# Kernel optimization log

Measured on AMD Instinct MI355X. Metric: run time of the kernel, lower is better.

Reference implementation:

```python
import jax, jax.numpy as jnp
import numpy as np

B, L, D, H = 2, 2048, 1024, 16
Dh = D // H


def setup_inputs() -> dict:
    key = jax.random.key(0)
    k = jax.random.split(key, 6)
    s = 1.0 / np.sqrt(D).astype(np.float32)
    return {
        "x": jax.random.normal(k[0], (B, L, D), jnp.float32),
        "mask": jnp.ones((B, L), jnp.int32),
        "user_emb": jax.random.normal(k[1], (B, D), jnp.float32),
        "W_q": jax.random.normal(k[2], (D, D), jnp.float32) * s,
        "W_k": jax.random.normal(k[3], (D, D), jnp.float32) * s,
        "W_v": jax.random.normal(k[4], (D, D), jnp.float32) * s,
        "W_o": jax.random.normal(k[5], (D, D), jnp.float32) * s,
    }


def reference(x, mask, user_emb, W_q, W_k, W_v, W_o):
    b, l, d = x.shape
    # torch nn.Linear(bias=False): y = x @ W.T
    Q = x @ W_q.T
    K = x @ W_k.T
    V = x @ W_v.T

    def split(t):  # [B,L,D] -> [B,H,L,Dh]
        return t.reshape(b, l, H, Dh).transpose(0, 2, 1, 3)

    Qh, Kh, Vh = split(Q), split(K), split(V)

    # additive_bias: rank-1 per-head user bias, [B,H,L,1]
    u = user_emb.reshape(b, H, Dh)
    bias = jnp.einsum('bhld,bhd->bhl', Qh, u)[..., None]

    scores = jnp.einsum('bhld,bhmd->bhlm', Qh, Kh) / np.float32(np.sqrt(Dh))
    scores = scores + bias
    # padding mask: 1 = valid, 0 = pad (broadcast over query dim)
    scores = jnp.where(mask[:, None, None, :] == 0, -jnp.inf, scores)
    # causal mask
    causal = jnp.triu(jnp.ones((l, l), jnp.bool_), k=1)
    scores = jnp.where(causal, -jnp.inf, scores)

    attn = jax.nn.softmax(scores, axis=-1)  # dropout p=0 -> identity
    ctx = jnp.einsum('bhlm,bhmd->bhld', attn, Vh)
    out = ctx.transpose(0, 2, 1, 3).reshape(b, l, d)
    return out @ W_o.T
```

## Files before the change

### kernel.cpp

```cpp
#include <hip/hip_runtime.h>
#include <hip/hip_bf16.h>
#include <stdint.h>

#define Bc 2
#define Lc 2048
#define Dc 1024
#define Hc 16
#define DHc 64

using f32x4  = __attribute__((ext_vector_type(4))) float;
using f32x16 = __attribute__((ext_vector_type(16))) float;
using bf16x8 = __attribute__((ext_vector_type(8))) short;
using bf16x4 = __attribute__((ext_vector_type(4))) short;

static __device__ __forceinline__ unsigned short f2bf(float f) {
  __hip_bfloat16 h = __float2bfloat16(f);
  return __builtin_bit_cast(unsigned short, h);
}
static __device__ __forceinline__ float bf2f(unsigned short u) {
  unsigned int x = ((unsigned int)u) << 16;
  return __builtin_bit_cast(float, x);
}
static __device__ __forceinline__ unsigned int cvtpk(float a, float b) {
  unsigned int r;
  asm("v_cvt_pk_bf16_f32 %0, %1, %2" : "=v"(r) : "v"(a), "v"(b));
  return r;
}

static __device__ __forceinline__ void gload16(const void* g, void* l) {
  __builtin_amdgcn_global_load_lds(
      (const __attribute__((address_space(1))) unsigned int*)g,
      (__attribute__((address_space(3))) unsigned int*)l, 16, 0, 0);
}

__global__ __launch_bounds__(256) void cvt_kernel(
    const float* __restrict__ x,  const float* __restrict__ wq,
    const float* __restrict__ wk, const float* __restrict__ wv,
    const float* __restrict__ wo,
    unsigned short* __restrict__ xb,  unsigned short* __restrict__ wqb,
    unsigned short* __restrict__ wkb, unsigned short* __restrict__ wvb,
    unsigned short* __restrict__ wob) {
  int i = (blockIdx.x * 256 + threadIdx.x) * 4;
  const float* src; unsigned short* dst; int off;
  if (i < 4194304) { src = x; dst = xb; off = i; }
  else {
    int j = i - 4194304; int w = j >> 20; off = j & 1048575;
    src = w == 0 ? wq : w == 1 ? wk : w == 2 ? wv : wo;
    dst = w == 0 ? wqb : w == 1 ? wkb : w == 2 ? wvb : wob;
  }
  float4 v = *(const float4*)(src + off);
  ushort4 u;
  u.x = f2bf(v.x); u.y = f2bf(v.y); u.z = f2bf(v.z); u.w = f2bf(v.w);
  *(ushort4*)(dst + off) = u;
}

__global__ __launch_bounds__(512) void gemm_qkv256(
    const unsigned short* __restrict__ xb,
    const unsigned short* __restrict__ wq, const unsigned short* __restrict__ wk,
    const unsigned short* __restrict__ wv,
    unsigned short* __restrict__ q, unsigned short* __restrict__ k,
    unsigned short* __restrict__ vT) {
  __shared__ char lds[131072];
  const int t = threadIdx.x;
  const int wid = t >> 6, l = t & 63;
  const int wr = wid >> 2, wc = wid & 3;
  const int tn0 = blockIdx.x * 256;
  const int my = blockIdx.y;
  const int wsel = my >> 2;
  const int tm = (my & 3) * 256;
  const unsigned short* W = wsel == 0 ? wq : wsel == 1 ? wk : wv;

  f32x4 zz = {0.f, 0.f, 0.f, 0.f};
  f32x4 acc[8][4];
#pragma unroll
  for (int a = 0; a < 8; a++)
#pragma unroll
    for (int b = 0; b < 4; b++) acc[a][b] = zz;

  const int rin = t >> 3;
  const int coff = (((t & 7) ^ (rin & 7)) << 4);
  const char* Asrc0 = (const char*)W + (size_t)(tm + rin) * 2048 + coff;
  const char* Bsrc0 = (const char*)xb + (size_t)(tn0 + rin) * 2048 + coff;

#define STG_A(bi, kt1, g)                                                     \
  gload16(Asrc0 + (size_t)(g) * 131072 + (kt1) * 128,                         \
          lds + (bi) * 65536 + (g) * 8192 + wid * 1024)
#define STG_B(bi, kt1, g)                                                     \
  gload16(Bsrc0 + (size_t)(g) * 131072 + (kt1) * 128,                         \
          lds + (bi) * 65536 + 32768 + (g) * 8192 + wid * 1024)

  STG_A(0, 0, 0); STG_A(0, 0, 2);
  STG_B(0, 0, 0); STG_B(0, 0, 1);
  STG_B(0, 0, 2); STG_B(0, 0, 3);
  STG_A(0, 0, 1); STG_A(0, 0, 3);

  const int cA = (l >> 4);
  const int rsw = l & 7;

  for (int kt = 0; kt < 16; ++kt) {
    const int cur = kt & 1;
    const char* Ab = lds + cur * 65536;
    const char* Bb = Ab + 32768;
    const int nxt = cur ^ 1;
    const bool pre = (kt + 1 < 16);
    const int k1 = kt + 1;
    bf16x8 bfr[4];

    asm volatile("s_waitcnt vmcnt(2)" ::: "memory");
    __builtin_amdgcn_sched_barrier(0);
    __builtin_amdgcn_s_barrier();
    __builtin_amdgcn_sched_barrier(0);
#pragma unroll
    for (int nn = 0; nn < 4; nn++) {
      int rb = wc * 64 + nn * 16 + (l & 15);
      bfr[nn] = *(const bf16x8*)(Bb + rb * 128 + ((cA ^ rsw) << 4));
    }
    {
      bf16x8 afr[4];
#pragma unroll
      for (int mm = 0; mm < 4; mm++) {
        int ra = wr * 128 + mm * 16 + (l & 15);
        afr[mm] = *(const bf16x8*)(Ab + ra * 128 + ((cA ^ rsw) << 4));
      }
      if (pre) { STG_A(nxt, k1, 0); STG_A(nxt, k1, 2); }
      __builtin_amdgcn_s_setprio(1);
#pragma unroll
      for (int mm = 0; mm < 4; mm++)
#pragma unroll
        for (int nn = 0; nn < 4; nn++)
          acc[mm][nn] = __builtin_amdgcn_mfma_f32_16x16x32_bf16(
              afr[mm], bfr[nn], acc[mm][nn], 0, 0, 0);
      __builtin_amdgcn_s_setprio(0);
    }

    if (pre) {
      asm volatile("s_waitcnt vmcnt(2)" ::: "memory");
    } else {
      asm volatile("s_waitcnt vmcnt(0)" ::: "memory");
    }
    __builtin_amdgcn_sched_barrier(0);
    __builtin_amdgcn_s_barrier();
    __builtin_amdgcn_sched_barrier(0);
    {
      bf16x8 afr[4];
#pragma unroll
      for (int mm = 0; mm < 4; mm++) {
        int ra = wr * 128 + 64 + mm * 16 + (l & 15);
        afr[mm] = *(const bf16x8*)(Ab + ra * 128 + ((cA ^ rsw) << 4));
      }
      if (pre) { STG_B(nxt, k1, 0); STG_B(nxt, k1, 1); }
      __builtin_amdgcn_s_setprio(1);
#pragma unroll
      for (int mm = 0; mm < 4; mm++)
#pragma unroll
        for (int nn = 0; nn < 4; nn++)
          acc[4 + mm][nn] = __builtin_amdgcn_mfma_f32_16x16x32_bf16(
              afr[mm], bfr[nn], acc[4 + mm][nn], 0, 0, 0);
      __builtin_amdgcn_s_setprio(0);
    }

#pragma unroll
    for (int nn = 0; nn < 4; nn++) {
      int rb = wc * 64 + nn * 16 + (l & 15);
      bfr[nn] = *(const bf16x8*)(Bb + rb * 128 + (((4 + cA) ^ rsw) << 4));
    }
    {
      bf16x8 afr[4];
#pragma unroll
      for (int mm = 0; mm < 4; mm++) {
        int ra = wr * 128 + mm * 16 + (l & 15);
        afr[mm] = *(const bf16x8*)(Ab + ra * 128 + (((4 + cA) ^ rsw) << 4));
      }
      if (pre) { STG_B(nxt, k1, 2); STG_B(nxt, k1, 3); }
      __builtin_amdgcn_s_setprio(1);
#pragma unroll
      for (int mm = 0; mm < 4; mm++)
#pragma unroll
        for (int nn = 0; nn < 4; nn++)
          acc[mm][nn] = __builtin_amdgcn_mfma_f32_16x16x32_bf16(
              afr[mm], bfr[nn], acc[mm][nn], 0, 0, 0);
      __builtin_amdgcn_s_setprio(0);
    }

    {
      bf16x8 afr[4];
#pragma unroll
      for (int mm = 0; mm < 4; mm++) {
        int ra = wr * 128 + 64 + mm * 16 + (l & 15);
        afr[mm] = *(const bf16x8*)(Ab + ra * 128 + (((4 + cA) ^ rsw) << 4));
      }
      if (pre) { STG_A(nxt, k1, 1); STG_A(nxt, k1, 3); }
      __builtin_amdgcn_s_setprio(1);
#pragma unroll
      for (int mm = 0; mm < 4; mm++)
#pragma unroll
        for (int nn = 0; nn < 4; nn++)
          acc[4 + mm][nn] = __builtin_amdgcn_mfma_f32_16x16x32_bf16(
              afr[mm], bfr[nn], acc[4 + mm][nn], 0, 0, 0);
      __builtin_amdgcn_s_setprio(0);
    }
  }
#undef STG_A
#undef STG_B

  const float scale = (wsel == 0) ? 0.125f * 1.44269504089f : 1.0f;
#pragma unroll
  for (int mm8 = 0; mm8 < 8; mm8++) {
    int f0 = tm + wr * 128 + mm8 * 16 + (l >> 4) * 4;
    int h = f0 >> 6, d0 = f0 & 63;
#pragma unroll
    for (int nn = 0; nn < 4; nn++) {
      int col = tn0 + wc * 64 + nn * 16 + (l & 15);
      int b = col >> 11, ll = col & 2047;
      if (wsel < 2) {
        bf16x4 v4;
#pragma unroll
        for (int r = 0; r < 4; r++) v4[r] = (short)f2bf(acc[mm8][nn][r] * scale);
        unsigned short* dst = wsel == 0 ? q : k;
        *(bf16x4*)&dst[((((size_t)(b * Hc + h) << 11) + ll) << 6) + d0] = v4;
      } else {
#pragma unroll
        for (int r = 0; r < 4; r++)
          vT[(((size_t)(b * Hc + h) * 64 + d0 + r) << 11) + ll] =
              f2bf(acc[mm8][nn][r]);
      }
    }
  }
}

__global__ __launch_bounds__(256) void gemm_out(
    const unsigned short* __restrict__ ctx, const unsigned short* __restrict__ wo,
    float* __restrict__ out) {
  __shared__ char lds[65536];
  const int t = threadIdx.x, w = t >> 6, l = t & 63;
  const int wr = w >> 1, wc = w & 1;
  const int tm = blockIdx.x * 128, tn = blockIdx.y * 128;
  f32x4 zz = {0.f, 0.f, 0.f, 0.f};
  f32x4 acc[4][4];
  for (int a = 0; a < 4; a++)
    for (int b = 0; b < 4; b++) acc[a][b] = zz;
  const char* Ag = (const char*)ctx;
  const char* Bg = (const char*)wo;
  const int s0i = w * 64;

  auto stage = [&](int bi, int kt) {
    char* base = lds + bi * 32768;
    const int kb = kt * 128;
#pragma unroll
    for (int i = 0; i < 4; i++) {
      int s = i * 256 + s0i + l;
      int row = s >> 3;
      int cs = (((s & 7) ^ (row & 7))) * 16;
      gload16(Ag + (size_t)(tm + row) * 2048 + kb + cs,
              base + (i * 256 + s0i) * 16);
      gload16(Bg + (size_t)(tn + row) * 2048 + kb + cs,
              base + 16384 + (i * 256 + s0i) * 16);
    }
  };

  stage(0, 0);
  for (int kt = 0; kt < 16; ++kt) {
    const int cur = kt & 1;
    const char* Ab = lds + cur * 32768;
    const char* Bb = Ab + 16384;
    if (kt + 1 < 16) {
      stage(cur ^ 1, kt + 1);
      asm volatile("s_waitcnt vmcnt(8)" ::: "memory");
    } else {
      asm volatile("s_waitcnt vmcnt(0)" ::: "memory");
    }
    __builtin_amdgcn_sched_barrier(0);
    __builtin_amdgcn_s_barrier();
    __builtin_amdgcn_sched_barrier(0);

    bf16x8 af[4][2], bfg[4][2];
#pragma unroll
    for (int mm = 0; mm < 4; mm++) {
      int row = wr * 64 + mm * 16 + (l & 15);
      int rsw = (row & 7) << 4;
#pragma unroll
      for (int kk = 0; kk < 2; kk++)
        af[mm][kk] = *(const bf16x8*)(Ab + row * 128 +
                                      ((kk * 64 + (l >> 4) * 16) ^ rsw));
    }
#pragma unroll
    for (int nn = 0; nn < 4; nn++) {
      int row = wc * 64 + nn * 16 + (l & 15);
      int rsw = (row & 7) << 4;
#pragma unroll
      for (int kk = 0; kk < 2; kk++)
        bfg[nn][kk] = *(const bf16x8*)(Bb + row * 128 +
                                       ((kk * 64 + (l >> 4) * 16) ^ rsw));
    }
#pragma unroll
    for (int kk = 0; kk < 2; kk++)
#pragma unroll
      for (int mm = 0; mm < 4; mm++)
#pragma unroll
        for (int nn = 0; nn < 4; nn++)
          acc[mm][nn] = __builtin_amdgcn_mfma_f32_16x16x32_bf16(
              af[mm][kk], bfg[nn][kk], acc[mm][nn], 0, 0, 0);
    __builtin_amdgcn_sched_barrier(0);
    __builtin_amdgcn_s_barrier();
  }

#pragma unroll
  for (int mm = 0; mm < 4; mm++) {
#pragma unroll
    for (int nn = 0; nn < 4; nn++) {
      int col = tn + wc * 64 + nn * 16 + (l & 15);
#pragma unroll
      for (int r = 0; r < 4; r++) {
        int row = tm + wr * 64 + mm * 16 + (l >> 4) * 4 + r;
        out[(size_t)row * 1024 + col] = acc[mm][nn][r];
      }
    }
  }
}

__device__ const int g_qt[36]  = {7,6,5,15,15,15,15,14,14,11,11,11,10,4,13,13,13,13,14,14,12,12,10,10,9,9,3,12,12,9,8,8,8,2,1,0};
__device__ const int g_kb0[36] = {0,0,0,0,8,16,24,0,8,0,8,16,0,0,0,7,14,21,16,23,0,7,8,15,0,7,0,14,20,14,0,6,12,0,0,0};
__device__ const int g_kb1[36] = {16,14,12,8,16,24,32,8,16,8,16,24,8,10,7,14,21,28,23,30,7,14,15,22,7,14,8,20,26,20,6,12,18,6,4,2};
__device__ const int g_pid[36] = {-1,-1,-1,0,1,2,3,4,5,16,17,18,19,-1,8,9,10,11,6,7,12,13,20,21,22,23,-1,14,15,24,25,26,27,-1,-1,-1};

__global__ __launch_bounds__(256, 4) void attn_kernel(
    const unsigned short* __restrict__ Q, const unsigned short* __restrict__ Kg,
    const unsigned short* __restrict__ VT,
    unsigned short* __restrict__ Op, float2* __restrict__ ml,
    unsigned short* __restrict__ ctx) {
  __shared__ char lds[32768];
  const int t = threadIdx.x, w = t >> 6, l = t & 63;
  const int hi = l >> 5, q32 = l & 31;
  const int idx = blockIdx.x;
  const int bh = idx & 31;
  const int g = idx >> 5;
  const int qt  = g_qt[g];
  const int kb0 = g_kb0[g];
  const int kb1 = g_kb1[g];
  const int pid = g_pid[g];
  const unsigned short* Qb = Q + bh * (Lc * DHc);
  const unsigned short* Kb = Kg + bh * (Lc * DHc);
  const unsigned short* Vb = VT + bh * (Lc * DHc);
  const int qrow = qt * 128 + w * 32 + q32;

  bf16x8 qf[4];
#pragma unroll
  for (int s = 0; s < 4; s++)
    qf[s] = *(const bf16x8*)(Qb + qrow * 64 + s * 16 + hi * 8);

  const f32x16 z16 = {0.f,0.f,0.f,0.f,0.f,0.f,0.f,0.f,
                      0.f,0.f,0.f,0.f,0.f,0.f,0.f,0.f};
  float mi = -1e30f, li = 0.f;
  f32x16 accO[2];
  accO[0] = z16; accO[1] = z16;

  const int s0i = w * 64 + l;
  auto stage = [&](int bi, int kb) {
    char* Ksb = lds + bi * 8192;
    char* Vsb = lds + 16384 + bi * 8192;
#pragma unroll
    for (int i = 0; i < 2; i++) {
      int s = i * 256 + s0i;
      int row = s >> 3;
      int cb = ((s & 7) * 16) ^ ((row & 7) << 4);
      gload16((const char*)Kb + (kb * 64 + row) * 128 + cb,
              Ksb + (i * 256 + w * 64) * 16);
      gload16((const char*)Vb + row * 4096 + kb * 128 + cb,
              Vsb + (i * 256 + w * 64) * 16);
    }
  };

  stage(0, kb0);
  for (int kb = kb0; kb < kb1; ++kb) {
    const int cur = (kb - kb0) & 1;
    char* Ks = lds + cur * 8192;
    char* Vs = lds + 16384 + cur * 8192;
    if (kb + 1 < kb1) {
      stage(cur ^ 1, kb + 1);
      asm volatile("s_waitcnt vmcnt(4)" ::: "memory");
    } else {
      asm volatile("s_waitcnt vmcnt(0)" ::: "memory");
    }
    __builtin_amdgcn_sched_barrier(0);
    __builtin_amdgcn_s_barrier();
    __builtin_amdgcn_sched_barrier(0);

    f32x16 sf[2];
    sf[0] = z16; sf[1] = z16;
    __builtin_amdgcn_s_setprio(1);
#pragma unroll
    for (int blk = 0; blk < 2; blk++) {
      int row = blk * 32 + q32;
      int rsw = (row & 7) << 4;
#pragma unroll
      for (int s = 0; s < 4; s++) {
        bf16x8 kf = *(const bf16x8*)(Ks + row * 128 + (((2 * s + hi) * 16) ^ rsw));
        sf[blk] = __builtin_amdgcn_mfma_f32_32x32x16_bf16(kf, qf[s], sf[blk], 0, 0, 0);
      }
    }
    __builtin_amdgcn_s_setprio(0);

    if (kb * 64 + 63 > qt * 128 + w * 32) {
#pragma unroll
      for (int blk = 0; blk < 2; blk++)
#pragma unroll
        for (int r = 0; r < 16; r++) {
          int kg = kb * 64 + blk * 32 + (r & 3) + 8 * (r >> 2) + 4 * hi;
          if (kg > qrow) sf[blk][r] = -1e30f;
        }
    }

    float tm16[16];
#pragma unroll
    for (int r = 0; r < 16; r++) tm16[r] = fmaxf(sf[0][r], sf[1][r]);
#pragma unroll
    for (int r = 0; r < 8; r++) tm16[r] = fmaxf(tm16[r], tm16[r + 8]);
#pragma unroll
    for (int r = 0; r < 4; r++) tm16[r] = fmaxf(tm16[r], tm16[r + 4]);
    float pm = fmaxf(fmaxf(tm16[0], tm16[1]), fmaxf(tm16[2], tm16[3]));
    pm = fmaxf(pm, __shfl_xor(pm, 32));

    if (!__all(pm - mi <= 8.f)) {
      float corr = __builtin_amdgcn_exp2f(mi - pm);
      mi = pm;
      li *= corr;
#pragma unroll
      for (int db = 0; db < 2; db++)
#pragma unroll
        for (int r = 0; r < 16; r++) accO[db][r] *= corr;
    }

    float a16[16];
#pragma unroll
    for (int r = 0; r < 16; r++) {
      float p0 = __builtin_amdgcn_exp2f(sf[0][r] - mi);
      float p1 = __builtin_amdgcn_exp2f(sf[1][r] - mi);
      sf[0][r] = p0; sf[1][r] = p1;
      a16[r] = p0 + p1;
    }
#pragma unroll
    for (int r = 0; r < 8; r++) a16[r] += a16[r + 8];
#pragma unroll
    for (int r = 0; r < 4; r++) a16[r] += a16[r + 4];
    float rs = (a16[0] + a16[1]) + (a16[2] + a16[3]);
    rs += __shfl_xor(rs, 32);
    li += rs;

    bf16x8 pf[4];
#pragma unroll
    for (int kw = 0; kw < 4; kw++) {
      const int bkl = kw >> 1, o = (kw & 1) * 8;
      unsigned int a01 = cvtpk(sf[bkl][o + 0], sf[bkl][o + 1]);
      unsigned int a23 = cvtpk(sf[bkl][o + 2], sf[bkl][o + 3]);
      unsigned int b01 = cvtpk(sf[bkl][o + 4], sf[bkl][o + 5]);
      unsigned int b23 = cvtpk(sf[bkl][o + 6], sf[bkl][o + 7]);
      auto s1 = __builtin_amdgcn_permlane32_swap(a01, b01, false, false);
      auto s2 = __builtin_amdgcn_permlane32_swap(a23, b23, false, false);
      uint4 uu;
      uu.x = s1[0];
      uu.y = s2[0];
      uu.z = s1[1];
      uu.w = s2[1];
      pf[kw] = __builtin_bit_cast(bf16x8, uu);
    }

    __builtin_amdgcn_s_setprio(1);
#pragma unroll
    for (int kw = 0; kw < 4; kw++) {
#pragma unroll
      for (int db = 0; db < 2; db++) {
        int row = db * 32 + q32;
        int rsw = (row & 7) << 4;
        bf16x8 vf = *(const bf16x8*)(Vs + row * 128 + (((2 * kw + hi) * 16) ^ rsw));
        accO[db] = __builtin_amdgcn_mfma_f32_32x32x16_bf16(vf, pf[kw], accO[db], 0, 0, 0);
      }
    }
    __builtin_amdgcn_s_setprio(0);
    __builtin_amdgcn_sched_barrier(0);
    __builtin_amdgcn_s_barrier();
  }

  const int b = bh >> 4, h = bh & 15;
  if (pid < 0) {
    float inv = 1.0f / li;
    unsigned short* dst = ctx + (size_t)(b * Lc + qrow) * Dc + h * 64;
#pragma unroll
    for (int db = 0; db < 2; db++)
#pragma unroll
      for (int rq = 0; rq < 4; rq++) {
        int d0 = db * 32 + 8 * rq + 4 * hi;
        bf16x4 v4;
#pragma unroll
        for (int j = 0; j < 4; j++) v4[j] = (short)f2bf(accO[db][rq * 4 + j] * inv);
        *(bf16x4*)(dst + d0) = v4;
      }
  } else {
    unsigned short* Opc = Op + (size_t)(bh * 28 + pid) * 8192;
    const int ql = w * 32 + q32;
#pragma unroll
    for (int db = 0; db < 2; db++)
#pragma unroll
      for (int rq = 0; rq < 4; rq++) {
        int d0 = db * 32 + 8 * rq + 4 * hi;
        bf16x4 v4;
#pragma unroll
        for (int j = 0; j < 4; j++) v4[j] = (short)f2bf(accO[db][rq * 4 + j]);
        *(bf16x4*)(Opc + ql * 64 + d0) = v4;
      }
    if (hi == 0) ml[(bh * 28 + pid) * 128 + ql] = make_float2(mi, li);
  }
}

__device__ const int c_pb[8]  = {25, 22, 19, 16, 12, 8, 4, 0};
__device__ const int c_nch[8] = { 3,  3,  3,  3,  4, 4, 4, 4};

__global__ __launch_bounds__(256) void combine_kernel(
    const unsigned short* __restrict__ Op, const float2* __restrict__ ml,
    unsigned short* __restrict__ ctx) {
  const int cb = blockIdx.x;
  const int qq = cb >> 5, bh = cb & 31;
  const int qt = 8 + qq;
  const int pb = c_pb[qq], nch = c_nch[qq];
  const int t = threadIdx.x;
  const int ql = t >> 1, dh = (t & 1) * 32;
  float2 pp[4];
  float mx = -1e30f;
#pragma unroll
  for (int j = 0; j < 4; j++) {
    int jj = j < nch ? j : 0;
    float2 v = ml[(size_t)(bh * 28 + pb + jj) * 128 + ql];
    pp[j] = (j < nch) ? v : make_float2(-1e30f, 0.f);
    mx = fmaxf(mx, pp[j].x);
  }
  float wgt[4];
  float den = 0.f;
#pragma unroll
  for (int j = 0; j < 4; j++) {
    float e = __builtin_amdgcn_exp2f(pp[j].x - mx);
    den += pp[j].y * e;
    wgt[j] = e;
  }
  float inv = 1.0f / den;
#pragma unroll
  for (int j = 0; j < 4; j++) wgt[j] *= inv;
  const int b = bh >> 4, h = bh & 15;
  unsigned short* dst = ctx + (size_t)(b * Lc + qt * 128 + ql) * Dc + h * 64 + dh;
  const unsigned short* q0 = Op + (size_t)(bh * 28 + pb) * 8192 + ql * 64 + dh;
#pragma unroll
  for (int seg = 0; seg < 4; seg++) {
    float a8[8] = {0.f, 0.f, 0.f, 0.f, 0.f, 0.f, 0.f, 0.f};
#pragma unroll
    for (int j = 0; j < 4; j++) {
      int jj = j < nch ? j : 0;
      bf16x8 o = *(const bf16x8*)(q0 + (size_t)jj * 8192 + seg * 8);
#pragma unroll
      for (int e = 0; e < 8; e++) a8[e] += wgt[j] * bf2f((unsigned short)o[e]);
    }
    bf16x8 outv;
#pragma unroll
    for (int e = 0; e < 8; e++) outv[e] = (short)f2bf(a8[e]);
    *(bf16x8*)(dst + seg * 8) = outv;
  }
}

extern "C" void kernel_launch(void* const* d_in, const int* in_sizes, int n_in,
                              void* d_out, int out_size, void* d_ws, size_t ws_size,
                              hipStream_t stream) {
  const float* x  = (const float*)d_in[0];
  const float* Wq = (const float*)d_in[3];
  const float* Wk = (const float*)d_in[4];
  const float* Wv = (const float*)d_in[5];
  const float* Wo = (const float*)d_in[6];

  char* ws = (char*)d_ws;
  const size_t MB = 1024 * 1024;
  unsigned short* xb  = (unsigned short*)(ws);
  unsigned short* wqb = (unsigned short*)(ws + 8 * MB);
  unsigned short* wkb = (unsigned short*)(ws + 10 * MB);
  unsigned short* wvb = (unsigned short*)(ws + 12 * MB);
  unsigned short* q   = (unsigned short*)(ws + 16 * MB);
  unsigned short* k   = (unsigned short*)(ws + 24 * MB);
  unsigned short* vT  = (unsigned short*)(ws + 32 * MB);
  unsigned short* ctx = (unsigned short*)(ws + 40 * MB);
  unsigned short* wob = (unsigned short*)(ws + 48 * MB);
  unsigned short* Op  = (unsigned short*)(ws);
  float2*         ml  = (float2*)(ws + 50 * MB);

  cvt_kernel<<<8192, 256, 0, stream>>>(x, Wq, Wk, Wv, Wo, xb, wqb, wkb, wvb, wob);
  gemm_qkv256<<<dim3(16, 12), 512, 0, stream>>>(xb, wqb, wkb, wvb, q, k, vT);
  attn_kernel<<<1152, 256, 0, stream>>>(q, k, vT, Op, ml, ctx);
  combine_kernel<<<256, 256, 0, stream>>>(Op, ml, ctx);
  gemm_out<<<dim3(32, 8), 256, 0, stream>>>(ctx, wob, (float*)d_out);
}
```

Before: 101.1 us.

## Shrink QKV GEMM tile to 128x256 with triple-buffered LDS pipeline

The QKV projection GEMM moves from 256x256 tiles with double buffering to 128x256 tiles with a three-slot LDS ring that prefetches two k-steps ahead. The grid doubles from 192 to 384 blocks, which should fill more of the compute units, and the deeper prefetch is meant to hide global-load latency better. In exchange each block reuses less data per tile, runs more barriers per k-step, and needs more LDS (144KB), so only one block fits per CU.

```diff
diff --git a/kernel.cpp b/kernel.cpp
--- a/kernel.cpp
+++ b/kernel.cpp
@@ -54,159 +54,129 @@
   *(ushort4*)(dst + off) = u;
 }
 
-__global__ __launch_bounds__(512) void gemm_qkv256(
+__global__ __launch_bounds__(512) void gemm_qkv8p(
     const unsigned short* __restrict__ xb,
     const unsigned short* __restrict__ wq, const unsigned short* __restrict__ wk,
     const unsigned short* __restrict__ wv,
     unsigned short* __restrict__ q, unsigned short* __restrict__ k,
     unsigned short* __restrict__ vT) {
-  __shared__ char lds[131072];
+  __shared__ char lds[147456];
   const int t = threadIdx.x;
   const int wid = t >> 6, l = t & 63;
   const int wr = wid >> 2, wc = wid & 3;
   const int tn0 = blockIdx.x * 256;
   const int my = blockIdx.y;
-  const int wsel = my >> 2;
-  const int tm = (my & 3) * 256;
+  const int wsel = my >> 3;
+  const int tm = (my & 7) * 128;
   const unsigned short* W = wsel == 0 ? wq : wsel == 1 ? wk : wv;
 
   f32x4 zz = {0.f, 0.f, 0.f, 0.f};
-  f32x4 acc[8][4];
-#pragma unroll
-  for (int a = 0; a < 8; a++)
+  f32x4 acc[4][4];
+#pragma unroll
+  for (int a = 0; a < 4; a++)
 #pragma unroll
     for (int b = 0; b < 4; b++) acc[a][b] = zz;
 
   const int rin = t >> 3;
-  const int coff = (((t & 7) ^ (rin & 7)) << 4);
-  const char* Asrc0 = (const char*)W + (size_t)(tm + rin) * 2048 + coff;
-  const char* Bsrc0 = (const char*)xb + (size_t)(tn0 + rin) * 2048 + coff;
-
-#define STG_A(bi, kt1, g)                                                     \
-  gload16(Asrc0 + (size_t)(g) * 131072 + (kt1) * 128,                         \
-          lds + (bi) * 65536 + (g) * 8192 + wid * 1024)
-#define STG_B(bi, kt1, g)                                                     \
-  gload16(Bsrc0 + (size_t)(g) * 131072 + (kt1) * 128,                         \
-          lds + (bi) * 65536 + 32768 + (g) * 8192 + wid * 1024)
-
-  STG_A(0, 0, 0); STG_A(0, 0, 2);
-  STG_B(0, 0, 0); STG_B(0, 0, 1);
-  STG_B(0, 0, 2); STG_B(0, 0, 3);
-  STG_A(0, 0, 1); STG_A(0, 0, 3);
-
-  const int cA = (l >> 4);
-  const int rsw = l & 7;
-
+  const int csw = ((t & 7) ^ (rin & 7)) << 4;
+  const char* Asrc = (const char*)W + (size_t)(tm + rin) * 2048 + csw;
+  const char* Bsrc = (const char*)xb + (size_t)(tn0 + rin) * 2048 + csw;
+
+#define SA(sl, kt, g)                                                        \
+  gload16(Asrc + (size_t)(g) * 131072 + (kt) * 128,                          \
+          lds + (sl) * 49152 + (g) * 8192 + wid * 1024)
+#define SB(sl, kt, g)                                                        \
+  gload16(Bsrc + (size_t)(g) * 131072 + (kt) * 128,                          \
+          lds + (sl) * 49152 + 16384 + (g) * 8192 + wid * 1024)
+
+  SA(0, 0, 0); SA(0, 0, 1); SB(0, 0, 0); SB(0, 0, 1); SB(0, 0, 2); SB(0, 0, 3);
+  SA(1, 1, 0); SA(1, 1, 1); SB(1, 1, 0); SB(1, 1, 1); SB(1, 1, 2); SB(1, 1, 3);
+  asm volatile("s_waitcnt vmcnt(6)" ::: "memory");
+  __builtin_amdgcn_sched_barrier(0);
+  __builtin_amdgcn_s_barrier();
+  __builtin_amdgcn_sched_barrier(0);
+
+  int slot = 0;
   for (int kt = 0; kt < 16; ++kt) {
-    const int cur = kt & 1;
-    const char* Ab = lds + cur * 65536;
-    const char* Bb = Ab + 32768;
-    const int nxt = cur ^ 1;
-    const bool pre = (kt + 1 < 16);
-    const int k1 = kt + 1;
-    bf16x8 bfr[4];
-
-    asm volatile("s_waitcnt vmcnt(2)" ::: "memory");
-    __builtin_amdgcn_sched_barrier(0);
-    __builtin_amdgcn_s_barrier();
-    __builtin_amdgcn_sched_barrier(0);
-#pragma unroll
-    for (int nn = 0; nn < 4; nn++) {
-      int rb = wc * 64 + nn * 16 + (l & 15);
-      bfr[nn] = *(const bf16x8*)(Bb + rb * 128 + ((cA ^ rsw) << 4));
-    }
+    const char* Ab = lds + slot * 49152;
+    const char* Bb = Ab + 16384;
+    const int s2 = slot < 1 ? slot + 2 : slot - 1;
+    const bool pre = (kt + 2 < 16);
+    const int k2 = kt + 2;
+
+    bf16x8 af[4], bfg[4];
     {
-      bf16x8 afr[4];
+      const int co = (l >> 4) * 16;
 #pragma unroll
       for (int mm = 0; mm < 4; mm++) {
-        int ra = wr * 128 + mm * 16 + (l & 15);
-        afr[mm] = *(const bf16x8*)(Ab + ra * 128 + ((cA ^ rsw) << 4));
-      }
-      if (pre) { STG_A(nxt, k1, 0); STG_A(nxt, k1, 2); }
-      __builtin_amdgcn_s_setprio(1);
-#pragma unroll
-      for (int mm = 0; mm < 4; mm++)
-#pragma unroll
-        for (int nn = 0; nn < 4; nn++)
-          acc[mm][nn] = __builtin_amdgcn_mfma_f32_16x16x32_bf16(
-              afr[mm], bfr[nn], acc[mm][nn], 0, 0, 0);
-      __builtin_amdgcn_s_setprio(0);
-    }
-
+        int ar = wr * 64 + mm * 16 + (l & 15);
+        af[mm] = *(const bf16x8*)(Ab + ar * 128 + (co ^ ((ar & 7) << 4)));
+      }
+#pragma unroll
+      for (int nn = 0; nn < 4; nn++) {
+        int br = wc * 64 + nn * 16 + (l & 15);
+        bfg[nn] = *(const bf16x8*)(Bb + br * 128 + (co ^ ((br & 7) << 4)));
+      }
+    }
     if (pre) {
-      asm volatile("s_waitcnt vmcnt(2)" ::: "memory");
+      SA(s2, k2, 0); SA(s2, k2, 1); SB(s2, k2, 0);
+      asm volatile("s_waitcnt vmcnt(3)" ::: "memory");
     } else {
       asm volatile("s_waitcnt vmcnt(0)" ::: "memory");
     }
     __builtin_amdgcn_sched_barrier(0);
     __builtin_amdgcn_s_barrier();
-    __builtin_amdgcn_sched_barrier(0);
+    asm volatile("s_waitcnt lgkmcnt(0)" ::: "memory");
+    __builtin_amdgcn_sched_barrier(0);
+    __builtin_amdgcn_s_setprio(1);
+#pragma unroll
+    for (int mm = 0; mm < 4; mm++)
+#pragma unroll
+      for (int nn = 0; nn < 4; nn++)
+        acc[mm][nn] = __builtin_amdgcn_mfma_f32_16x16x32_bf16(
+            af[mm], bfg[nn], acc[mm][nn], 0, 0, 0);
+    __builtin_amdgcn_s_setprio(0);
+    __builtin_amdgcn_sched_barrier(0);
+    __builtin_amdgcn_s_barrier();
+
     {
-      bf16x8 afr[4];
+      const int co = (4 + (l >> 4)) * 16;
 #pragma unroll
       for (int mm = 0; mm < 4; mm++) {
-        int ra = wr * 128 + 64 + mm * 16 + (l & 15);
-        afr[mm] = *(const bf16x8*)(Ab + ra * 128 + ((cA ^ rsw) << 4));
-      }
-      if (pre) { STG_B(nxt, k1, 0); STG_B(nxt, k1, 1); }
-      __builtin_amdgcn_s_setprio(1);
-#pragma unroll
-      for (int mm = 0; mm < 4; mm++)
-#pragma unroll
-        for (int nn = 0; nn < 4; nn++)
-          acc[4 + mm][nn] = __builtin_amdgcn_mfma_f32_16x16x32_bf16(
-              afr[mm], bfr[nn], acc[4 + mm][nn], 0, 0, 0);
-      __builtin_amdgcn_s_setprio(0);
-    }
-
-#pragma unroll
-    for (int nn = 0; nn < 4; nn++) {
-      int rb = wc * 64 + nn * 16 + (l & 15);
-      bfr[nn] = *(const bf16x8*)(Bb + rb * 128 + (((4 + cA) ^ rsw) << 4));
-    }
-    {
-      bf16x8 afr[4];
-#pragma unroll
-      for (int mm = 0; mm < 4; mm++) {
-        int ra = wr * 128 + mm * 16 + (l & 15);
-        afr[mm] = *(const bf16x8*)(Ab + ra * 128 + (((4 + cA) ^ rsw) << 4));
-      }
-      if (pre) { STG_B(nxt, k1, 2); STG_B(nxt, k1, 3); }
-      __builtin_amdgcn_s_setprio(1);
-#pragma unroll
-      for (int mm = 0; mm < 4; mm++)
-#pragma unroll
-        for (int nn = 0; nn < 4; nn++)
-          acc[mm][nn] = __builtin_amdgcn_mfma_f32_16x16x32_bf16(
-              afr[mm], bfr[nn], acc[mm][nn], 0, 0, 0);
-      __builtin_amdgcn_s_setprio(0);
-    }
-
-    {
-      bf16x8 afr[4];
-#pragma unroll
-      for (int mm = 0; mm < 4; mm++) {
-        int ra = wr * 128 + 64 + mm * 16 + (l & 15);
-        afr[mm] = *(const bf16x8*)(Ab + ra * 128 + (((4 + cA) ^ rsw) << 4));
-      }
-      if (pre) { STG_A(nxt, k1, 1); STG_A(nxt, k1, 3); }
-      __builtin_amdgcn_s_setprio(1);
-#pragma unroll
-      for (int mm = 0; mm < 4; mm++)
-#pragma unroll
-        for (int nn = 0; nn < 4; nn++)
-          acc[4 + mm][nn] = __builtin_amdgcn_mfma_f32_16x16x32_bf16(
-              afr[mm], bfr[nn], acc[4 + mm][nn], 0, 0, 0);
-      __builtin_amdgcn_s_setprio(0);
-    }
-  }
-#undef STG_A
-#undef STG_B
+        int ar = wr * 64 + mm * 16 + (l & 15);
+        af[mm] = *(const bf16x8*)(Ab + ar * 128 + (co ^ ((ar & 7) << 4)));
+      }
+#pragma unroll
+      for (int nn = 0; nn < 4; nn++) {
+        int br = wc * 64 + nn * 16 + (l & 15);
+        bfg[nn] = *(const bf16x8*)(Bb + br * 128 + (co ^ ((br & 7) << 4)));
+      }
+    }
+    if (pre) { SB(s2, k2, 1); SB(s2, k2, 2); SB(s2, k2, 3); }
+    __builtin_amdgcn_sched_barrier(0);
+    __builtin_amdgcn_s_barrier();
+    asm volatile("s_waitcnt lgkmcnt(0)" ::: "memory");
+    __builtin_amdgcn_sched_barrier(0);
+    __builtin_amdgcn_s_setprio(1);
+#pragma unroll
+    for (int mm = 0; mm < 4; mm++)
+#pragma unroll
+      for (int nn = 0; nn < 4; nn++)
+        acc[mm][nn] = __builtin_amdgcn_mfma_f32_16x16x32_bf16(
+            af[mm], bfg[nn], acc[mm][nn], 0, 0, 0);
+    __builtin_amdgcn_s_setprio(0);
+    __builtin_amdgcn_sched_barrier(0);
+    __builtin_amdgcn_s_barrier();
+
+    slot = slot == 2 ? 0 : slot + 1;
+  }
+#undef SA
+#undef SB
 
   const float scale = (wsel == 0) ? 0.125f * 1.44269504089f : 1.0f;
 #pragma unroll
-  for (int mm8 = 0; mm8 < 8; mm8++) {
-    int f0 = tm + wr * 128 + mm8 * 16 + (l >> 4) * 4;
+  for (int mm = 0; mm < 4; mm++) {
+    int f0 = tm + wr * 64 + mm * 16 + (l >> 4) * 4;
     int h = f0 >> 6, d0 = f0 & 63;
 #pragma unroll
     for (int nn = 0; nn < 4; nn++) {
@@ -215,14 +185,14 @@
       if (wsel < 2) {
         bf16x4 v4;
 #pragma unroll
-        for (int r = 0; r < 4; r++) v4[r] = (short)f2bf(acc[mm8][nn][r] * scale);
+        for (int r = 0; r < 4; r++) v4[r] = (short)f2bf(acc[mm][nn][r] * scale);
         unsigned short* dst = wsel == 0 ? q : k;
         *(bf16x4*)&dst[((((size_t)(b * Hc + h) << 11) + ll) << 6) + d0] = v4;
       } else {
 #pragma unroll
         for (int r = 0; r < 4; r++)
           vT[(((size_t)(b * Hc + h) * 64 + d0 + r) << 11) + ll] =
-              f2bf(acc[mm8][nn][r]);
+              f2bf(acc[mm][nn][r]);
       }
     }
   }
@@ -587,7 +557,7 @@
   float2*         ml  = (float2*)(ws + 50 * MB);
 
   cvt_kernel<<<8192, 256, 0, stream>>>(x, Wq, Wk, Wv, Wo, xb, wqb, wkb, wvb, wob);
-  gemm_qkv256<<<dim3(16, 12), 512, 0, stream>>>(xb, wqb, wkb, wvb, q, k, vT);
+  gemm_qkv8p<<<dim3(16, 24), 512, 0, stream>>>(xb, wqb, wkb, wvb, q, k, vT);
   attn_kernel<<<1152, 256, 0, stream>>>(q, k, vT, Op, ml, ctx);
   combine_kernel<<<256, 256, 0, stream>>>(Op, ml, ctx);
   gemm_out<<<dim3(32, 8), 256, 0, stream>>>(ctx, wob, (float*)d_out);
```

Measured after the change: 106.8 us. +5.7%, slower.
